# Kernel tuning notes

Measured on AMD Instinct MI355X. Metric: run time of the kernel, lower is better.

The kernel has to match this reference:

```python
import jax, jax.numpy as jnp
import numpy as np

STRIDE = (1, 1)
PADDING = (1, 1)
DILATION = (1, 1)


def deform_conv(x, offset, weight, stride=STRIDE, padding=PADDING, dilation=DILATION):
    """Deformable convolution v1 (mmcv layout), deformable_groups=1, groups=1.

    x:      [B, C, H, W]
    offset: [B, 2*kh*kw, Ho, Wo]   pairs ordered (dy, dx) per kernel tap
    weight: [Co, C, kh, kw]
    """
    B, C, H, W = x.shape
    Co, Ci, kh, kw = weight.shape
    sh, sw = stride
    ph, pw = padding
    dh, dw = dilation
    Ho = (H + 2 * ph - (dh * (kh - 1) + 1)) // sh + 1
    Wo = (W + 2 * pw - (dw * (kw - 1) + 1)) // sw + 1
    K2 = kh * kw

    off = offset.reshape(B, K2, 2, Ho, Wo)
    # base sampling grid per kernel tap: [K2, Ho, Wo]
    ky = (jnp.arange(K2) // kw) * dh          # kernel row offsets
    kx = (jnp.arange(K2) % kw) * dw           # kernel col offsets
    hi = jnp.arange(Ho) * sh - ph             # output-row -> input-row base
    wi = jnp.arange(Wo) * sw - pw
    py = off[:, :, 0] + (ky[:, None, None] + hi[None, :, None])  # [B,K2,Ho,Wo]
    px = off[:, :, 1] + (kx[:, None, None] + wi[None, None, :])  # [B,K2,Ho,Wo]

    y0 = jnp.floor(py)
    x0 = jnp.floor(px)
    ly = py - y0
    lx = px - x0
    hy = 1.0 - ly
    hx = 1.0 - lx
    y0i = y0.astype(jnp.int32)
    x0i = x0.astype(jnp.int32)
    y1i = y0i + 1
    x1i = x0i + 1

    xf = x.reshape(B, C, H * W)

    def gather(yi, xi):
        # zero padding outside the image, per-corner validity (DCN semantics)
        valid = (yi >= 0) & (yi < H) & (xi >= 0) & (xi < W)
        yc = jnp.clip(yi, 0, H - 1)
        xc = jnp.clip(xi, 0, W - 1)
        idx = (yc * W + xc).reshape(B, -1)                 # [B, K2*Ho*Wo]
        vals = jax.vmap(lambda xb, ib: xb[:, ib])(xf, idx)  # [B, C, K2*Ho*Wo]
        vals = vals.reshape(B, C, K2, Ho, Wo)
        return vals * valid[:, None].astype(x.dtype)

    # im2col with bilinear sampling: [B, C, K2, Ho, Wo]
    col = (gather(y0i, x0i) * (hy * hx)[:, None]
           + gather(y0i, x1i) * (hy * lx)[:, None]
           + gather(y1i, x0i) * (ly * hx)[:, None]
           + gather(y1i, x1i) * (ly * lx)[:, None])

    # GEMM: out[b,o,h,w] = sum_{c,k} W[o,c,k] * col[b,c,k,h,w]
    out = jnp.einsum('bckhw,ock->bohw', col, weight.reshape(Co, Ci, K2))
    return out


def setup_inputs() -> dict:
    key = jax.random.key(0)
    k1, k2, k3 = jax.random.split(key, 3)
    x = jax.random.normal(k1, (4, 256, 64, 64), dtype=jnp.float32)
    offset = jax.random.normal(k2, (4, 18, 64, 64), dtype=jnp.float32)
    n = 256 * 3 * 3
    stdv = 1.0 / np.sqrt(n)
    weight = jax.random.uniform(k3, (256, 256, 3, 3), dtype=jnp.float32,
                                minval=-stdv, maxval=stdv)
    return {"x": x, "offset": offset, "weight": weight}


def reference(x, offset, weight):
    return deform_conv(x, offset, weight)
```

## Files before the change

### kernel.cpp

```cpp
#include <hip/hip_runtime.h>
#include <hip/hip_bf16.h>
#include <cstddef>

#define B_    4
#define C_    256
#define H_    64
#define W_    64
#define CO_   256
#define K2_   9
#define NSTEP 72

typedef __attribute__((ext_vector_type(8))) short short8;
typedef __attribute__((ext_vector_type(4))) float f32x4;

__device__ __forceinline__ unsigned short f2bf(float f) {
    unsigned u = __builtin_bit_cast(unsigned, f);
    u = (u + 0x7fffu + ((u >> 16) & 1u)) >> 16;
    return (unsigned short)u;
}
__device__ __forceinline__ unsigned pack2bf(float lo, float hi) {
    __hip_bfloat162 h = __float22bfloat162_rn(make_float2(lo, hi));
    unsigned r; __builtin_memcpy(&r, &h, 4);
    return r;
}
__device__ __forceinline__ float bflo(unsigned u) {
    return __builtin_bit_cast(float, u << 16);
}
__device__ __forceinline__ float bfhi(unsigned u) {
    return __builtin_bit_cast(float, u & 0xffff0000u);
}

#if defined(__has_builtin)
#if __has_builtin(__builtin_amdgcn_fdot2_f32_bf16)
#define HAS_BFDOT2 1
#endif
#endif
__device__ __forceinline__ float dot2bf(unsigned x, unsigned w, float acc) {
#ifdef HAS_BFDOT2
    typedef __attribute__((ext_vector_type(2))) __bf16 bf16x2;
    return __builtin_amdgcn_fdot2_f32_bf16(__builtin_bit_cast(bf16x2, x),
                                           __builtin_bit_cast(bf16x2, w),
                                           acc, false);
#else
    return acc + bflo(x) * bflo(w) + bfhi(x) * bfhi(w);
#endif
}

__global__ void wpack_kernel(const float* __restrict__ w,
                             unsigned short* __restrict__ wpk) {
    const int idx = blockIdx.x * 256 + threadIdx.x;
    if (idx >= NSTEP * 16 * 64) return;
    const int lane = idx & 63;
    const int mt   = (idx >> 6) & 15;
    const int s    = idx >> 10;
    const int o    = mt * 16 + (lane & 15);
    const int cc   = s / 9;
    const int t    = s - 9 * cc;
    const int c0   = cc * 32 + ((lane >> 4) << 3);
    unsigned short h[8];
#pragma unroll
    for (int e = 0; e < 8; ++e)
        h[e] = f2bf(w[(o * C_ + c0 + e) * K2_ + t]);
    uint4 v;
    v.x = h[0] | ((unsigned)h[1] << 16);
    v.y = h[2] | ((unsigned)h[3] << 16);
    v.z = h[4] | ((unsigned)h[5] << 16);
    v.w = h[6] | ((unsigned)h[7] << 16);
    *reinterpret_cast<uint4*>(&wpk[(size_t)idx * 8]) = v;
}

__device__ __forceinline__ short8 loadA(const unsigned short* __restrict__ wpk,
                                        const float* __restrict__ wraw,
                                        int use_pk, int s, int mt, int lane) {
    if (use_pk) {
        return *reinterpret_cast<const short8*>(
            wpk + (((size_t)(s * 16 + mt) * 64 + lane) << 3));
    } else {
        const int cc = s / 9;
        const int t  = s - 9 * cc;
        const int c0 = cc * 32 + ((lane >> 4) << 3);
        const int o  = mt * 16 + (lane & 15);
        short8 r;
#pragma unroll
        for (int e = 0; e < 8; ++e)
            r[e] = (short)f2bf(wraw[(o * C_ + c0 + e) * K2_ + t]);
        return r;
    }
}

__global__ __launch_bounds__(512, 4)
void dcn_mfma_kernel(const float* __restrict__ x,
                     const float* __restrict__ off,
                     const unsigned short* __restrict__ wpk,
                     const float* __restrict__ wraw,
                     float* __restrict__ out,
                     int use_pk) {
    __shared__ __align__(16) unsigned s_win[32 * 484 + 48];
    __shared__ __align__(8)  unsigned s_mwp[K2_ * 32 * 2];
    __shared__ int s_menc[K2_ * 32];
    __shared__ __align__(16) unsigned short s_colb[2][3][1024];

    const int tid = threadIdx.x;
    const int bid = blockIdx.x;
    const int xcd  = bid & 7;
    const int slot = bid >> 3;
    const int b    = xcd >> 1;
    const int ho   = ((xcd & 1) << 5) | (slot >> 1);
    const int woh  = slot & 1;
    const int wo0  = woh << 5;

    const char* xb8 = (const char*)x + ((size_t)b << 22);

    if (tid < 48) s_win[32 * 484 + tid] = 0u;

    if (tid < K2_ * 32) {
        const int t = tid >> 5;
        const int p = tid & 31;
        const int pa = wo0 + p;
        const float dy = off[((b * 18 + 2 * t    ) * 64 + ho) * 64 + pa];
        const float dx = off[((b * 18 + 2 * t + 1) * 64 + ho) * 64 + pa];
        const float py = (float)(ho - 1 + t / 3) + dy;
        const float px = (float)(pa - 1 + t % 3) + dx;
        const float y0f = floorf(py), x0f = floorf(px);
        const float ly = py - y0f, lx = px - x0f;
        const float hy = 1.0f - ly, hx = 1.0f - lx;
        const int y0 = (int)y0f, x0 = (int)x0f;
        const int y1 = y0 + 1,   x1 = x0 + 1;
        const bool vy0 = (y0 >= 0) & (y0 < H_);
        const bool vy1 = (y1 >= 0) & (y1 < H_);
        const bool vx0 = (x0 >= 0) & (x0 < W_);
        const bool vx1 = (x1 >= 0) & (x1 < W_);
        const int yc0 = min(max(y0, 0), H_ - 1);
        const int yc1 = min(max(y1, 0), H_ - 1);
        const int xc0 = min(max(x0, 0), W_ - 1);
        const int xc1 = min(max(x1, 0), W_ - 1);
        float w00 = (vy0 && vx0) ? hy * hx : 0.0f;
        float w01 = (vy0 && vx1) ? hy * lx : 0.0f;
        float w10 = (vy1 && vx0) ? ly * hx : 0.0f;
        float w11 = (vy1 && vx1) ? ly * lx : 0.0f;
        const int dys = yc1 - yc0, dxs = xc1 - xc0;
        if (!dxs) { w00 += w01; w01 = 0.0f; w10 += w11; w11 = 0.0f; }
        if (!dys) { w00 += w10; w10 = 0.0f; w01 += w11; w11 = 0.0f; }
        const int r0 = yc0 - (ho - 5);
        const int j0 = xc0 - (wo0 - 8);
        const bool fast = (r0 >= 0) & (r0 + dys <= 10) & (j0 >= 0) & (j0 <= 43);
        int enc;
        if (fast)
            enc = (r0 * 44 + j0) << 2;
        else
            enc = (int)(0x80000000u
                        | (unsigned)((((yc0 << 6) + xc0) << 2) | (dys << 1) | dxs));
        s_mwp[(t * 32 + p) * 2    ] = pack2bf(w00, w01);
        s_mwp[(t * 32 + p) * 2 + 1] = pack2bf(w10, w11);
        s_menc[t * 32 + p] = enc;
    }

    unsigned stoff[8];
#pragma unroll
    for (int v = 0; v < 8; ++v) {
        const int u = tid + (v << 9);
        if (u < 3872) {
            const int cl  = u / 121;
            const int rem = u - cl * 121;
            const int r   = rem / 11;
            const int q   = rem - r * 11;
            const int y   = ho - 5 + r;
            int gof = (((y << 6) + wo0 - 8) << 2) + (q << 4);
            gof = min(max(gof, 0), 16368);
            if ((unsigned)y >= 64u) gof = 0;
            stoff[v] = ((unsigned)cl << 14) + (unsigned)gof;
        } else {
            stoff[v] = 0xffffffffu;
        }
    }

    const int lane = tid & 63;
    const int wave = tid >> 6;
    const int wo   = lane & 31;
    const int kk0  = (wave << 2) | ((lane >> 5) << 1);
    const unsigned swr = ((unsigned)(wo >> 4) << 10)
                       | ((unsigned)((wo & 15) | ((kk0 >> 3) << 4)) << 4)
                       | ((unsigned)(kk0 & 7) << 1);
    const unsigned brd = (unsigned)lane << 4;
    const int mt0 = wave << 1;
    const char* winC = (const char*)s_win + kk0 * 1936;
    const char* winD = winC + 1936;

    f32x4 acc[2][2];
#pragma unroll
    for (int m = 0; m < 2; ++m)
#pragma unroll
        for (int nt = 0; nt < 2; ++nt)
            acc[m][nt] = (f32x4)(0.0f);

#define STAGEW(XCB_) do {                                                      \
        char* wb_ = (char*)s_win + (size_t)tid * 16;                           \
        _Pragma("unroll")                                                      \
        for (int v_ = 0; v_ < 8; ++v_) {                                       \
            const unsigned so_ = stoff[v_];                                    \
            if (so_ != 0xffffffffu) {                                          \
                const float4 g_ = *(const float4*)((XCB_) + so_);              \
                const unsigned in_ = so_ & 16383u;                             \
                const float g4_ = *(const float*)((XCB_)                       \
                                    + (in_ >= 16368u ? so_ : so_ + 16));       \
                uint4 pk_;                                                     \
                pk_.x = pack2bf(g_.x, g_.y);                                   \
                pk_.y = pack2bf(g_.y, g_.z);                                   \
                pk_.z = pack2bf(g_.z, g_.w);                                   \
                pk_.w = pack2bf(g_.w, g4_);                                    \
                *(uint4*)(wb_ + v_ * 8192) = pk_;                              \
            }                                                                  \
        }                                                                      \
    } while (0)

#define COLT1(T_, DST_, XCB_) do {                                             \
        const unsigned u01_ = s_mwp[((T_) * 32 + wo) * 2];                     \
        const unsigned u23_ = s_mwp[((T_) * 32 + wo) * 2 + 1];                 \
        const int mb_ = s_menc[(T_) * 32 + wo];                                \
        float vA_, vB_;                                                        \
        if (__builtin_expect(mb_ >= 0, 1)) {                                   \
            const char* pA_ = winC + mb_;                                      \
            const char* pB_ = winD + mb_;                                      \
            const unsigned a0_ = *(const unsigned*)(pA_);                      \
            const unsigned a1_ = *(const unsigned*)(pA_ + 176);                \
            const unsigned c0_ = *(const unsigned*)(pB_);                      \
            const unsigned c1_ = *(const unsigned*)(pB_ + 176);                \
            vA_ = dot2bf(a1_, u23_, dot2bf(a0_, u01_, 0.0f));                  \
            vB_ = dot2bf(c1_, u23_, dot2bf(c0_, u01_, 0.0f));                  \
        } else {                                                               \
            const float w0_ = bflo(u01_), w1_ = bfhi(u01_);                    \
            const float w2_ = bflo(u23_), w3_ = bfhi(u23_);                    \
            const int dxb_ = (mb_ & 1) << 2, dyb_ = (mb_ & 2) << 7;            \
            const int o_ = mb_ & 0x3fffc;                                      \
            const char* plA_ = (XCB_) + ((size_t)kk0 << 14);                   \
            const char* plB_ = plA_ + (1 << 14);                               \
            vA_ = w0_ * *(const float*)(plA_ + o_)                             \
                + w1_ * *(const float*)(plA_ + o_ + dxb_)                      \
                + w2_ * *(const float*)(plA_ + o_ + dyb_)                      \
                + w3_ * *(const float*)(plA_ + o_ + dyb_ + dxb_);              \
            vB_ = w0_ * *(const float*)(plB_ + o_)                             \
                + w1_ * *(const float*)(plB_ + o_ + dxb_)                      \
                + w2_ * *(const float*)(plB_ + o_ + dyb_)                      \
                + w3_ * *(const float*)(plB_ + o_ + dyb_ + dxb_);              \
        }                                                                      \
        *(unsigned*)((char*)(DST_) + swr) = pack2bf(vA_, vB_);                 \
    } while (0)

#define MFMA_(A_, B_, C_) __builtin_amdgcn_mfma_f32_16x16x32_bf16(A_, B_, C_, 0, 0, 0)

#define GEMM22(SLOT_, A0_, A1_) do {                                           \
        const char* cb_ = (const char*)(SLOT_);                                \
        const short8 b0_ = *(const short8*)(cb_ + brd);                        \
        const short8 b1_ = *(const short8*)(cb_ + brd + 1024);                 \
        acc[0][0] = MFMA_(A0_, b0_, acc[0][0]);                                \
        acc[0][1] = MFMA_(A0_, b1_, acc[0][1]);                                \
        acc[1][0] = MFMA_(A1_, b0_, acc[1][0]);                                \
        acc[1][1] = MFMA_(A1_, b1_, acc[1][1]);                                \
    } while (0)

#define BARLG() do {                                                           \
        asm volatile("s_waitcnt lgkmcnt(0)" ::: "memory");                     \
        __builtin_amdgcn_s_barrier();                                          \
    } while (0)

#define PHASE3(TC_, CDST_, TG_, GSRC_, XCB_) do {                              \
        const short8 a00_ = loadA(wpk, wraw, use_pk, s0 + (TG_),     mt0,     lane); \
        const short8 a01_ = loadA(wpk, wraw, use_pk, s0 + (TG_),     mt0 + 1, lane); \
        const short8 a10_ = loadA(wpk, wraw, use_pk, s0 + (TG_) + 1, mt0,     lane); \
        const short8 a11_ = loadA(wpk, wraw, use_pk, s0 + (TG_) + 1, mt0 + 1, lane); \
        const short8 a20_ = loadA(wpk, wraw, use_pk, s0 + (TG_) + 2, mt0,     lane); \
        const short8 a21_ = loadA(wpk, wraw, use_pk, s0 + (TG_) + 2, mt0 + 1, lane); \
        COLT1((TC_),     (char*)(CDST_),        XCB_);                         \
        COLT1((TC_) + 1, (char*)(CDST_) + 2048, XCB_);                         \
        COLT1((TC_) + 2, (char*)(CDST_) + 4096, XCB_);                         \
        GEMM22((char*)(GSRC_),        a00_, a01_);                             \
        GEMM22((char*)(GSRC_) + 2048, a10_, a11_);                             \
        GEMM22((char*)(GSRC_) + 4096, a20_, a21_);                             \
        BARLG();                                                               \
    } while (0)

    STAGEW(xb8);
    __syncthreads();
    COLT1(0, (char*)s_colb,        xb8);
    COLT1(1, (char*)s_colb + 2048, xb8);
    COLT1(2, (char*)s_colb + 4096, xb8);
    BARLG();

    for (int cc = 0; cc < 8; ++cc) {
        const char* xcb  = xb8 + ((size_t)cc << 19);
        const char* xcbN = xb8 + ((size_t)(cc + 1) << 19);
        char* bufP = (char*)s_colb + (cc & 1) * 6144;
        char* bufQ = (char*)s_colb + ((cc & 1) ^ 1) * 6144;
        const int s0 = cc * 9;

        PHASE3(3, bufQ, 0, bufP, xcb);

        PHASE3(6, bufP, 3, bufQ, xcb);

        {
            const short8 a00_ = loadA(wpk, wraw, use_pk, s0 + 6, mt0,     lane);
            const short8 a01_ = loadA(wpk, wraw, use_pk, s0 + 6, mt0 + 1, lane);
            const short8 a10_ = loadA(wpk, wraw, use_pk, s0 + 7, mt0,     lane);
            const short8 a11_ = loadA(wpk, wraw, use_pk, s0 + 7, mt0 + 1, lane);
            const short8 a20_ = loadA(wpk, wraw, use_pk, s0 + 8, mt0,     lane);
            const short8 a21_ = loadA(wpk, wraw, use_pk, s0 + 8, mt0 + 1, lane);
            if (cc < 7) STAGEW(xcbN);
            GEMM22(bufP,        a00_, a01_);
            GEMM22(bufP + 2048, a10_, a11_);
            GEMM22(bufP + 4096, a20_, a21_);
            BARLG();
        }

        if (cc < 7) {
            COLT1(0, bufQ,        xcbN);
            COLT1(1, bufQ + 2048, xcbN);
            COLT1(2, bufQ + 4096, xcbN);
            BARLG();
        }
    }

#undef STAGEW
#undef COLT1
#undef MFMA_
#undef GEMM22
#undef BARLG
#undef PHASE3

#pragma unroll
    for (int m = 0; m < 2; ++m) {
        const int ob = (mt0 + m) * 16 + ((lane >> 4) << 2);
#pragma unroll
        for (int r = 0; r < 4; ++r) {
            float* orow = out + (((size_t)(b * CO_ + ob + r) * 64 + ho) * 64 + wo0);
#pragma unroll
            for (int nt = 0; nt < 2; ++nt)
                orow[(nt << 4) | (lane & 15)] = acc[m][nt][r];
        }
    }
}

extern "C" void kernel_launch(void* const* d_in, const int* in_sizes, int n_in,
                              void* d_out, int out_size, void* d_ws, size_t ws_size,
                              hipStream_t stream) {
    const float* x      = (const float*)d_in[0];
    const float* offset = (const float*)d_in[1];
    const float* weight = (const float*)d_in[2];
    float* out = (float*)d_out;

    const size_t pk_bytes = (size_t)NSTEP * 16 * 64 * 8 * 2;
    const int use_pk = (ws_size >= pk_bytes) ? 1 : 0;
    unsigned short* wpk = (unsigned short*)d_ws;

    if (use_pk) {
        wpack_kernel<<<288, 256, 0, stream>>>(weight, wpk);
    }
    dcn_mfma_kernel<<<512, 512, 0, stream>>>(x, offset, wpk, weight, out, use_pk);
}
```

Before: 65.74 us.

## Halve output tile width to 16 columns and double grid size

Each block now covers 16 output columns instead of 32, so the grid grows from 512 to 1024 blocks and the shared window, column buffer and per-tap tables shrink. Each lane now samples a single channel and each wave issues one MFMA column tile instead of two. Launch bounds are raised to allow more resident blocks per CU. This aims to improve occupancy and load balance across CUs. In exchange, each x window row is staged more often, weight A-fragments are reloaded twice as often per output, and overlapping halo loads are duplicated across blocks.

```diff
diff --git a/kernel.cpp b/kernel.cpp
--- a/kernel.cpp
+++ b/kernel.cpp
@@ -88,34 +88,34 @@
     }
 }
 
-__global__ __launch_bounds__(512, 4)
+__global__ __launch_bounds__(512, 6)
 void dcn_mfma_kernel(const float* __restrict__ x,
                      const float* __restrict__ off,
                      const unsigned short* __restrict__ wpk,
                      const float* __restrict__ wraw,
                      float* __restrict__ out,
                      int use_pk) {
-    __shared__ __align__(16) unsigned s_win[32 * 484 + 48];
-    __shared__ __align__(8)  unsigned s_mwp[K2_ * 32 * 2];
-    __shared__ int s_menc[K2_ * 32];
-    __shared__ __align__(16) unsigned short s_colb[2][3][1024];
+    __shared__ __align__(16) unsigned s_win[32 * 308 + 48];
+    __shared__ __align__(8)  unsigned s_mwp[K2_ * 16 * 2];
+    __shared__ int s_menc[K2_ * 16];
+    __shared__ __align__(16) unsigned short s_colb[2][3][512];
 
     const int tid = threadIdx.x;
     const int bid = blockIdx.x;
     const int xcd  = bid & 7;
     const int slot = bid >> 3;
     const int b    = xcd >> 1;
-    const int ho   = ((xcd & 1) << 5) | (slot >> 1);
-    const int woh  = slot & 1;
-    const int wo0  = woh << 5;
+    const int ho   = ((xcd & 1) << 5) | (slot >> 2);
+    const int woq  = slot & 3;
+    const int wo0  = woq << 4;
 
     const char* xb8 = (const char*)x + ((size_t)b << 22);
 
-    if (tid < 48) s_win[32 * 484 + tid] = 0u;
-
-    if (tid < K2_ * 32) {
-        const int t = tid >> 5;
-        const int p = tid & 31;
+    if (tid < 48) s_win[32 * 308 + tid] = 0u;
+
+    if (tid < K2_ * 16) {
+        const int t = tid >> 4;
+        const int p = tid & 15;
         const int pa = wo0 + p;
         const float dy = off[((b * 18 + 2 * t    ) * 64 + ho) * 64 + pa];
         const float dx = off[((b * 18 + 2 * t + 1) * 64 + ho) * 64 + pa];
@@ -143,27 +143,27 @@
         if (!dys) { w00 += w10; w10 = 0.0f; w01 += w11; w11 = 0.0f; }
         const int r0 = yc0 - (ho - 5);
         const int j0 = xc0 - (wo0 - 8);
-        const bool fast = (r0 >= 0) & (r0 + dys <= 10) & (j0 >= 0) & (j0 <= 43);
+        const bool fast = (r0 >= 0) & (r0 + dys <= 10) & (j0 >= 0) & (j0 <= 27);
         int enc;
         if (fast)
-            enc = (r0 * 44 + j0) << 2;
+            enc = (r0 * 28 + j0) << 2;
         else
             enc = (int)(0x80000000u
                         | (unsigned)((((yc0 << 6) + xc0) << 2) | (dys << 1) | dxs));
-        s_mwp[(t * 32 + p) * 2    ] = pack2bf(w00, w01);
-        s_mwp[(t * 32 + p) * 2 + 1] = pack2bf(w10, w11);
-        s_menc[t * 32 + p] = enc;
-    }
-
-    unsigned stoff[8];
-#pragma unroll
-    for (int v = 0; v < 8; ++v) {
+        s_mwp[(t * 16 + p) * 2    ] = pack2bf(w00, w01);
+        s_mwp[(t * 16 + p) * 2 + 1] = pack2bf(w10, w11);
+        s_menc[t * 16 + p] = enc;
+    }
+
+    unsigned stoff[5];
+#pragma unroll
+    for (int v = 0; v < 5; ++v) {
         const int u = tid + (v << 9);
-        if (u < 3872) {
-            const int cl  = u / 121;
-            const int rem = u - cl * 121;
-            const int r   = rem / 11;
-            const int q   = rem - r * 11;
+        if (u < 2464) {
+            const int cl  = u / 77;
+            const int rem = u - cl * 77;
+            const int r   = rem / 7;
+            const int q   = rem - r * 7;
             const int y   = ho - 5 + r;
             int gof = (((y << 6) + wo0 - 8) << 2) + (q << 4);
             gof = min(max(gof, 0), 16368);
@@ -176,27 +176,22 @@
 
     const int lane = tid & 63;
     const int wave = tid >> 6;
-    const int wo   = lane & 31;
-    const int kk0  = (wave << 2) | ((lane >> 5) << 1);
-    const unsigned swr = ((unsigned)(wo >> 4) << 10)
-                       | ((unsigned)((wo & 15) | ((kk0 >> 3) << 4)) << 4)
-                       | ((unsigned)(kk0 & 7) << 1);
+    const int wo   = lane & 15;
+    const int kk   = (wave << 2) | (lane >> 4);
+    const unsigned swr = ((unsigned)(wo | ((kk >> 3) << 4)) << 4)
+                       | ((unsigned)(kk & 7) << 1);
     const unsigned brd = (unsigned)lane << 4;
     const int mt0 = wave << 1;
-    const char* winC = (const char*)s_win + kk0 * 1936;
-    const char* winD = winC + 1936;
-
-    f32x4 acc[2][2];
-#pragma unroll
-    for (int m = 0; m < 2; ++m)
-#pragma unroll
-        for (int nt = 0; nt < 2; ++nt)
-            acc[m][nt] = (f32x4)(0.0f);
+    const char* winC = (const char*)s_win + kk * 1232;
+
+    f32x4 acc[2];
+#pragma unroll
+    for (int m = 0; m < 2; ++m) acc[m] = (f32x4)(0.0f);
 
 #define STAGEW(XCB_) do {                                                      \
         char* wb_ = (char*)s_win + (size_t)tid * 16;                           \
         _Pragma("unroll")                                                      \
-        for (int v_ = 0; v_ < 8; ++v_) {                                       \
+        for (int v_ = 0; v_ < 5; ++v_) {                                       \
             const unsigned so_ = stoff[v_];                                    \
             if (so_ != 0xffffffffu) {                                          \
                 const float4 g_ = *(const float4*)((XCB_) + so_);              \
@@ -214,48 +209,35 @@
     } while (0)
 
 #define COLT1(T_, DST_, XCB_) do {                                             \
-        const unsigned u01_ = s_mwp[((T_) * 32 + wo) * 2];                     \
-        const unsigned u23_ = s_mwp[((T_) * 32 + wo) * 2 + 1];                 \
-        const int mb_ = s_menc[(T_) * 32 + wo];                                \
-        float vA_, vB_;                                                        \
+        const unsigned u01_ = s_mwp[((T_) * 16 + wo) * 2];                     \
+        const unsigned u23_ = s_mwp[((T_) * 16 + wo) * 2 + 1];                 \
+        const int mb_ = s_menc[(T_) * 16 + wo];                                \
+        float vA_;                                                             \
         if (__builtin_expect(mb_ >= 0, 1)) {                                   \
             const char* pA_ = winC + mb_;                                      \
-            const char* pB_ = winD + mb_;                                      \
             const unsigned a0_ = *(const unsigned*)(pA_);                      \
-            const unsigned a1_ = *(const unsigned*)(pA_ + 176);                \
-            const unsigned c0_ = *(const unsigned*)(pB_);                      \
-            const unsigned c1_ = *(const unsigned*)(pB_ + 176);                \
+            const unsigned a1_ = *(const unsigned*)(pA_ + 112);                \
             vA_ = dot2bf(a1_, u23_, dot2bf(a0_, u01_, 0.0f));                  \
-            vB_ = dot2bf(c1_, u23_, dot2bf(c0_, u01_, 0.0f));                  \
         } else {                                                               \
             const float w0_ = bflo(u01_), w1_ = bfhi(u01_);                    \
             const float w2_ = bflo(u23_), w3_ = bfhi(u23_);                    \
             const int dxb_ = (mb_ & 1) << 2, dyb_ = (mb_ & 2) << 7;            \
             const int o_ = mb_ & 0x3fffc;                                      \
-            const char* plA_ = (XCB_) + ((size_t)kk0 << 14);                   \
-            const char* plB_ = plA_ + (1 << 14);                               \
+            const char* plA_ = (XCB_) + ((size_t)kk << 14);                    \
             vA_ = w0_ * *(const float*)(plA_ + o_)                             \
                 + w1_ * *(const float*)(plA_ + o_ + dxb_)                      \
                 + w2_ * *(const float*)(plA_ + o_ + dyb_)                      \
                 + w3_ * *(const float*)(plA_ + o_ + dyb_ + dxb_);              \
-            vB_ = w0_ * *(const float*)(plB_ + o_)                             \
-                + w1_ * *(const float*)(plB_ + o_ + dxb_)                      \
-                + w2_ * *(const float*)(plB_ + o_ + dyb_)                      \
-                + w3_ * *(const float*)(plB_ + o_ + dyb_ + dxb_);              \
         }                                                                      \
-        *(unsigned*)((char*)(DST_) + swr) = pack2bf(vA_, vB_);                 \
+        *(unsigned short*)((char*)(DST_) + swr) = f2bf(vA_);                   \
     } while (0)
 
 #define MFMA_(A_, B_, C_) __builtin_amdgcn_mfma_f32_16x16x32_bf16(A_, B_, C_, 0, 0, 0)
 
-#define GEMM22(SLOT_, A0_, A1_) do {                                           \
-        const char* cb_ = (const char*)(SLOT_);                                \
-        const short8 b0_ = *(const short8*)(cb_ + brd);                        \
-        const short8 b1_ = *(const short8*)(cb_ + brd + 1024);                 \
-        acc[0][0] = MFMA_(A0_, b0_, acc[0][0]);                                \
-        acc[0][1] = MFMA_(A0_, b1_, acc[0][1]);                                \
-        acc[1][0] = MFMA_(A1_, b0_, acc[1][0]);                                \
-        acc[1][1] = MFMA_(A1_, b1_, acc[1][1]);                                \
+#define GEMM21(SLOT_, A0_, A1_) do {                                           \
+        const short8 b0_ = *(const short8*)((const char*)(SLOT_) + brd);       \
+        acc[0] = MFMA_(A0_, b0_, acc[0]);                                      \
+        acc[1] = MFMA_(A1_, b0_, acc[1]);                                      \
     } while (0)
 
 #define BARLG() do {                                                           \
@@ -271,26 +253,26 @@
         const short8 a20_ = loadA(wpk, wraw, use_pk, s0 + (TG_) + 2, mt0,     lane); \
         const short8 a21_ = loadA(wpk, wraw, use_pk, s0 + (TG_) + 2, mt0 + 1, lane); \
         COLT1((TC_),     (char*)(CDST_),        XCB_);                         \
-        COLT1((TC_) + 1, (char*)(CDST_) + 2048, XCB_);                         \
-        COLT1((TC_) + 2, (char*)(CDST_) + 4096, XCB_);                         \
-        GEMM22((char*)(GSRC_),        a00_, a01_);                             \
-        GEMM22((char*)(GSRC_) + 2048, a10_, a11_);                             \
-        GEMM22((char*)(GSRC_) + 4096, a20_, a21_);                             \
+        COLT1((TC_) + 1, (char*)(CDST_) + 1024, XCB_);                         \
+        COLT1((TC_) + 2, (char*)(CDST_) + 2048, XCB_);                         \
+        GEMM21((char*)(GSRC_),        a00_, a01_);                             \
+        GEMM21((char*)(GSRC_) + 1024, a10_, a11_);                             \
+        GEMM21((char*)(GSRC_) + 2048, a20_, a21_);                             \
         BARLG();                                                               \
     } while (0)
 
     STAGEW(xb8);
     __syncthreads();
     COLT1(0, (char*)s_colb,        xb8);
-    COLT1(1, (char*)s_colb + 2048, xb8);
-    COLT1(2, (char*)s_colb + 4096, xb8);
+    COLT1(1, (char*)s_colb + 1024, xb8);
+    COLT1(2, (char*)s_colb + 2048, xb8);
     BARLG();
 
     for (int cc = 0; cc < 8; ++cc) {
         const char* xcb  = xb8 + ((size_t)cc << 19);
         const char* xcbN = xb8 + ((size_t)(cc + 1) << 19);
-        char* bufP = (char*)s_colb + (cc & 1) * 6144;
-        char* bufQ = (char*)s_colb + ((cc & 1) ^ 1) * 6144;
+        char* bufP = (char*)s_colb + (cc & 1) * 3072;
+        char* bufQ = (char*)s_colb + ((cc & 1) ^ 1) * 3072;
         const int s0 = cc * 9;
 
         PHASE3(3, bufQ, 0, bufP, xcb);
@@ -305,16 +287,16 @@
             const short8 a20_ = loadA(wpk, wraw, use_pk, s0 + 8, mt0,     lane);
             const short8 a21_ = loadA(wpk, wraw, use_pk, s0 + 8, mt0 + 1, lane);
             if (cc < 7) STAGEW(xcbN);
-            GEMM22(bufP,        a00_, a01_);
-            GEMM22(bufP + 2048, a10_, a11_);
-            GEMM22(bufP + 4096, a20_, a21_);
+            GEMM21(bufP,        a00_, a01_);
+            GEMM21(bufP + 1024, a10_, a11_);
+            GEMM21(bufP + 2048, a20_, a21_);
             BARLG();
         }
 
         if (cc < 7) {
             COLT1(0, bufQ,        xcbN);
-            COLT1(1, bufQ + 2048, xcbN);
-            COLT1(2, bufQ + 4096, xcbN);
+            COLT1(1, bufQ + 1024, xcbN);
+            COLT1(2, bufQ + 2048, xcbN);
             BARLG();
         }
     }
@@ -322,19 +304,17 @@
 #undef STAGEW
 #undef COLT1
 #undef MFMA_
-#undef GEMM22
+#undef GEMM21
 #undef BARLG
 #undef PHASE3
 
+    const int ncol = wo0 + wo;
 #pragma unroll
     for (int m = 0; m < 2; ++m) {
         const int ob = (mt0 + m) * 16 + ((lane >> 4) << 2);
 #pragma unroll
         for (int r = 0; r < 4; ++r) {
-            float* orow = out + (((size_t)(b * CO_ + ob + r) * 64 + ho) * 64 + wo0);
-#pragma unroll
-            for (int nt = 0; nt < 2; ++nt)
-                orow[(nt << 4) | (lane & 15)] = acc[m][nt][r];
+            out[(((size_t)(b * CO_ + ob + r) * 64 + ho) << 6) + ncol] = acc[m][r];
         }
     }
 }
@@ -354,5 +334,5 @@
     if (use_pk) {
         wpack_kernel<<<288, 256, 0, stream>>>(weight, wpk);
     }
-    dcn_mfma_kernel<<<512, 512, 0, stream>>>(x, offset, wpk, weight, out, use_pk);
-}
+    dcn_mfma_kernel<<<1024, 512, 0, stream>>>(x, offset, wpk, weight, out, use_pk);
+}
```

Result: slower. 102.3 us (+55.6%).
